# Optimization experiments

Measured on AMD Instinct MI355X. Metric: run time of the kernel, lower is better.

## Reference

```python
import jax, jax.numpy as jnp
import numpy as np

NUM_HEADS = 4
WINDOW_SIZE = 7
DILATION = 1


def local_mask(height, width, window_size, dilation):
    """[N, N] bool mask: True where token i may attend to token j (dilated 2D window)."""
    radius = window_size // 2
    rows = jnp.arange(height)
    cols = jnp.arange(width)
    r = jnp.repeat(rows, width)          # [N] row index of each flattened token
    c = jnp.tile(cols, height)           # [N] col index of each flattened token
    dr = r[:, None] - r[None, :]         # [N, N]
    dc = c[:, None] - c[None, :]
    within = (jnp.abs(dr) <= radius * dilation) & (jnpp_abs(dc) <= radius * dilation) if False else (
        (jnp.abs(dr) <= radius * dilation) & (jnp.abs(dc) <= radius * dilation)
    )
    on_grid = (dr % dilation == 0) & (dc % dilation == 0)
    return within & on_grid


def setup_inputs() -> dict:
    key = jax.random.key(0)
    kq, kk, kv = jax.random.split(key, 3)
    shape = (2, 64, 64, 64)  # (B, C, H, W)
    q = jax.random.normal(kq, shape, dtype=jnp.float32)
    k = jax.random.normal(kk, shape, dtype=jnp.float32)
    v = jax.random.normal(kv, shape, dtype=jnp.float32)
    return {"q": q, "k": k, "v": v}


def reference(q, k, v):
    B, C, H, W = q.shape
    nh = NUM_HEADS
    hd = C // nh
    N = H * W

    def to_seq(x):
        # (B, C, H, W) -> (B, nh, N, hd)
        x = x.reshape(B, nh, hd, H, W)
        return x.transpose(0, 1, 3, 4, 2).reshape(B, nh, N, hd)

    q_seq = to_seq(q)
    k_seq = to_seq(k)
    v_seq = to_seq(v)

    scale = 1.0 / jnp.sqrt(jnp.asarray(hd, dtype=q.dtype))
    scores = jnp.einsum("bhqd,bhkd->bhqk", q_seq, k_seq) * scale  # [B, nh, N, N]

    mask = local_mask(H, W, WINDOW_SIZE, DILATION)  # [N, N] bool
    neg = jnp.finfo(scores.dtype).min
    scores = jnp.where(mask[None, None, :, :], scores, neg)

    attn = jax.nn.softmax(scores, axis=-1)
    out = jnp.einsum("bhqk,bhkd->bhqd", attn, v_seq)  # [B, nh, N, hd]

    # (B, nh, N, hd) -> (B, C, H, W)
    out = out.reshape(B, nh, H, W, hd).transpose(0, 1, 4, 2, 3).reshape(B, C, H, W)
    return out
```

## Files before the change

kernel.cpp:

```cpp
#include <hip/hip_runtime.h>
#include <hip/hip_bf16.h>
#include <math.h>

#define HD  16
#define HW  4096
#define RAD 3

__global__ __launch_bounds__(256, 2)
void local_attn_kernel(const float* __restrict__ q,
                       const float* __restrict__ k,
                       const float* __restrict__ v,
                       float* __restrict__ out) {
    __shared__ float ldsK[7168];
    __shared__ float ldsV[7168];

    const int tid = threadIdx.x;
    const int c   = tid & 63;
    const int w   = tid >> 6;

    const int bid = blockIdx.x;
    const int r   = bid & 63;
    const int h   = (bid >> 6) & 3;
    const int b   = bid >> 8;
    const int base = (b * 4 + h) * (HD * HW);
    const int pos  = r * 64 + c;

#pragma unroll
    for (int ii = 0; ii < 7; ++ii) {
        int ci = w + ii * 4;
        int s  = ci * 4 + (c >> 4);
        int d  = (int)((unsigned)s / 7u);
        int lr = s - d * 7;
        int rr = r - RAD + lr;
        rr = rr < 0 ? 0 : (rr > 63 ? 63 : rr);
        int cc = (c & 15) * 4;
        const float* gk = k + base + d * HW + rr * 64 + cc;
        const float* gv = v + base + d * HW + rr * 64 + cc;
#if defined(__has_builtin) && __has_builtin(__builtin_amdgcn_global_load_lds)
        __builtin_amdgcn_global_load_lds(
            (const __attribute__((address_space(1))) void*)gk,
            (__attribute__((address_space(3))) void*)&ldsK[ci * 256], 16, 0, 0);
        __builtin_amdgcn_global_load_lds(
            (const __attribute__((address_space(1))) void*)gv,
            (__attribute__((address_space(3))) void*)&ldsV[ci * 256], 16, 0, 0);
#else
        *(float4*)&ldsK[ci * 256 + c * 4] = *(const float4*)gk;
        *(float4*)&ldsV[ci * 256 + c * 4] = *(const float4*)gv;
#endif
    }

    float qv[HD];
#pragma unroll
    for (int d = 0; d < HD; ++d)
        qv[d] = q[base + d * HW + pos] * 0.25f;

    int e2 = (c - RAD) & ~1;
    if (e2 < 0) e2 = 0;
    if (e2 > 56) e2 = 56;
    int lo = c - RAD; if (lo < 0) lo = 0;
    int hi = c + RAD; if (hi > 63) hi = 63;
    const int jlo = lo - e2, jhi = hi - e2;

    __syncthreads();

    float acc[HD];
#pragma unroll
    for (int d = 0; d < HD; ++d) acc[d] = 0.0f;
    float lsum = 0.0f;

#pragma unroll
    for (int t2 = 0; t2 < 2; ++t2) {
        const int dr = w + t2 * 4;
        const int rr = r - RAD + dr;
        if (dr < 7 && (unsigned)rr < 64u) {
            float s8[8];
#pragma unroll
            for (int j = 0; j < 8; ++j) s8[j] = 0.0f;
#pragma unroll
            for (int d = 0; d < HD; ++d) {
                const float* kr = &ldsK[d * 448 + dr * 64 + e2];
                float2 k0 = *(const float2*)(kr);
                float2 k1 = *(const float2*)(kr + 2);
                float2 k2 = *(const float2*)(kr + 4);
                float2 k3 = *(const float2*)(kr + 6);
                s8[0] = fmaf(qv[d], k0.x, s8[0]);
                s8[1] = fmaf(qv[d], k0.y, s8[1]);
                s8[2] = fmaf(qv[d], k1.x, s8[2]);
                s8[3] = fmaf(qv[d], k1.y, s8[3]);
                s8[4] = fmaf(qv[d], k2.x, s8[4]);
                s8[5] = fmaf(qv[d], k2.y, s8[5]);
                s8[6] = fmaf(qv[d], k3.x, s8[6]);
                s8[7] = fmaf(qv[d], k3.y, s8[7]);
            }
#pragma unroll
            for (int j = 0; j < 8; ++j) {
                float p = __expf(s8[j]);
                p = (j >= jlo && j <= jhi) ? p : 0.0f;
                s8[j] = p;
                lsum += p;
            }
#pragma unroll
            for (int d = 0; d < HD; ++d) {
                const float* vr = &ldsV[d * 448 + dr * 64 + e2];
                float2 v0 = *(const float2*)(vr);
                float2 v1 = *(const float2*)(vr + 2);
                float2 v2 = *(const float2*)(vr + 4);
                float2 v3 = *(const float2*)(vr + 6);
                float a = acc[d];
                a = fmaf(s8[0], v0.x, a);
                a = fmaf(s8[1], v0.y, a);
                a = fmaf(s8[2], v1.x, a);
                a = fmaf(s8[3], v1.y, a);
                a = fmaf(s8[4], v2.x, a);
                a = fmaf(s8[5], v2.y, a);
                a = fmaf(s8[6], v3.x, a);
                a = fmaf(s8[7], v3.y, a);
                acc[d] = a;
            }
        }
    }

    __syncthreads();
#pragma unroll
    for (int d = 0; d < HD; ++d)
        ldsK[d * 256 + w * 64 + c] = acc[d];
    ldsK[4096 + w * 64 + c] = lsum;
    __syncthreads();

    float lt = ldsK[4096 + c] + ldsK[4160 + c] + ldsK[4224 + c] + ldsK[4288 + c];
    float invl = 1.0f / lt;
#pragma unroll
    for (int i = 0; i < 4; ++i) {
        int d  = w * 4 + i;
        int a0 = d * 256 + c;
        float a = ldsK[a0] + ldsK[a0 + 64] + ldsK[a0 + 128] + ldsK[a0 + 192];
        out[base + d * HW + pos] = a * invl;
    }
}

extern "C" void kernel_launch(void* const* d_in, const int* in_sizes, int n_in,
                              void* d_out, int out_size, void* d_ws, size_t ws_size,
                              hipStream_t stream) {
    const float* q = (const float*)d_in[0];
    const float* k = (const float*)d_in[1];
    const float* v = (const float*)d_in[2];
    float* out = (float*)d_out;

    int queries = out_size / HD;
    int blocks  = queries / 64;
    local_attn_kernel<<<blocks, 256, 0, stream>>>(q, k, v, out);
}
```

Baseline: 12.02 us.

## Use 512 threads per block, one wave per window row

Doubles the block to 8 waves. Waves 0-3 load K and waves 4-7 load V into one shared LDS array, and each wave handles a single window row instead of two. The cross-wave reduction now sums 8 partial accumulators, and each wave writes 2 output channels. This is meant to raise parallelism and shorten each wave's serial work. In exchange the eighth wave does no compute, and the final reduction uses more LDS reads.

New measurement: 12.43 us. +3.4%, slower.

```diff
diff --git a/kernel.cpp b/kernel.cpp
--- a/kernel.cpp
+++ b/kernel.cpp
@@ -6,13 +6,14 @@
 #define HW  4096
 #define RAD 3
 
-__global__ __launch_bounds__(256, 2)
+__global__ __launch_bounds__(512, 4)
 void local_attn_kernel(const float* __restrict__ q,
                        const float* __restrict__ k,
                        const float* __restrict__ v,
                        float* __restrict__ out) {
-    __shared__ float ldsK[7168];
-    __shared__ float ldsV[7168];
+    __shared__ float lds[14336];
+    float* ldsK = lds;
+    float* ldsV = lds + 7168;
 
     const int tid = threadIdx.x;
     const int c   = tid & 63;
@@ -25,34 +26,35 @@
     const int base = (b * 4 + h) * (HD * HW);
     const int pos  = r * 64 + c;
 
+    {
+        const float* src = (w < 4) ? (k + base) : (v + base);
+        float* dst = (w < 4) ? ldsK : ldsV;
+        const int wl = w & 3;
 #pragma unroll
-    for (int ii = 0; ii < 7; ++ii) {
-        int ci = w + ii * 4;
-        int s  = ci * 4 + (c >> 4);
-        int d  = (int)((unsigned)s / 7u);
-        int lr = s - d * 7;
-        int rr = r - RAD + lr;
-        rr = rr < 0 ? 0 : (rr > 63 ? 63 : rr);
-        int cc = (c & 15) * 4;
-        const float* gk = k + base + d * HW + rr * 64 + cc;
-        const float* gv = v + base + d * HW + rr * 64 + cc;
+        for (int ii = 0; ii < 7; ++ii) {
+            int ci = wl + ii * 4;
+            int s  = ci * 4 + (c >> 4);
+            int d  = (int)((unsigned)s / 7u);
+            int lr = s - d * 7;
+            int rr = r - RAD + lr;
+            rr = rr < 0 ? 0 : (rr > 63 ? 63 : rr);
+            const float* g = src + d * HW + rr * 64 + (c & 15) * 4;
 #if defined(__has_builtin) && __has_builtin(__builtin_amdgcn_global_load_lds)
-        __builtin_amdgcn_global_load_lds(
-            (const __attribute__((address_space(1))) void*)gk,
-            (__attribute__((address_space(3))) void*)&ldsK[ci * 256], 16, 0, 0);
-        __builtin_amdgcn_global_load_lds(
-            (const __attribute__((address_space(1))) void*)gv,
-            (__attribute__((address_space(3))) void*)&ldsV[ci * 256], 16, 0, 0);
+            __builtin_amdgcn_global_load_lds(
+                (const __attribute__((address_space(1))) void*)g,
+                (__attribute__((address_space(3))) void*)&dst[ci * 256], 16, 0, 0);
 #else
-        *(float4*)&ldsK[ci * 256 + c * 4] = *(const float4*)gk;
-        *(float4*)&ldsV[ci * 256 + c * 4] = *(const float4*)gv;
+            *(float4*)&dst[ci * 256 + c * 4] = *(const float4*)g;
 #endif
+        }
     }
 
     float qv[HD];
+    if (w < 7) {
 #pragma unroll
-    for (int d = 0; d < HD; ++d)
-        qv[d] = q[base + d * HW + pos] * 0.25f;
+        for (int d = 0; d < HD; ++d)
+            qv[d] = q[base + d * HW + pos] * 0.25f;
+    }
 
     int e2 = (c - RAD) & ~1;
     if (e2 < 0) e2 = 0;
@@ -68,9 +70,8 @@
     for (int d = 0; d < HD; ++d) acc[d] = 0.0f;
     float lsum = 0.0f;
 
-#pragma unroll
-    for (int t2 = 0; t2 < 2; ++t2) {
-        const int dr = w + t2 * 4;
+    {
+        const int dr = w;
         const int rr = r - RAD + dr;
         if (dr < 7 && (unsigned)rr < 64u) {
             float s8[8];
@@ -123,17 +124,24 @@
     __syncthreads();
 #pragma unroll
     for (int d = 0; d < HD; ++d)
-        ldsK[d * 256 + w * 64 + c] = acc[d];
-    ldsK[4096 + w * 64 + c] = lsum;
+        lds[d * 512 + w * 64 + c] = acc[d];
+    lds[8192 + w * 64 + c] = lsum;
     __syncthreads();
 
-    float lt = ldsK[4096 + c] + ldsK[4160 + c] + ldsK[4224 + c] + ldsK[4288 + c];
-    float invl = 1.0f / lt;
+    float lt = 0.0f;
 #pragma unroll
-    for (int i = 0; i < 4; ++i) {
-        int d  = w * 4 + i;
-        int a0 = d * 256 + c;
-        float a = ldsK[a0] + ldsK[a0 + 64] + ldsK[a0 + 128] + ldsK[a0 + 192];
+    for (int s = 0; s < 8; ++s)
+        lt += lds[8192 + s * 64 + c];
+    const float invl = 1.0f / lt;
+
+#pragma unroll
+    for (int i = 0; i < 2; ++i) {
+        int d  = w * 2 + i;
+        int a0 = d * 512 + c;
+        float a = 0.0f;
+#pragma unroll
+        for (int s = 0; s < 8; ++s)
+            a += lds[a0 + s * 64];
         out[base + d * HW + pos] = a * invl;
     }
 }
@@ -148,5 +156,5 @@
 
     int queries = out_size / HD;
     int blocks  = queries / 64;
-    local_attn_kernel<<<blocks, 256, 0, stream>>>(q, k, v, out);
+    local_attn_kernel<<<blocks, 512, 0, stream>>>(q, k, v, out);
 }
```
